# Kernel tuning notes

Measured on AMD Instinct MI355X. Metric: run time of the kernel, lower is better.

The kernel has to match this reference:

```python
import jax, jax.numpy as jnp
import numpy as np

H = 64  # LSTM hidden size (from LSTM(64, ...))

def _lstm(xs, W, U, b, return_sequences):
    """Keras-convention LSTM. xs: [B, T, D]; W: [D, 4H]; U: [H, 4H]; b: [4H].
    Gate order i, f, g(candidate), o; sigmoid recurrent activation, tanh activation."""
    B = xs.shape[0]
    h_dim = U.shape[0]
    # Precompute input projection for all timesteps (hoists the big GEMM out of scan)
    xW = jnp.einsum('btd,dk->btk', xs, W) + b  # [B, T, 4H]

    def step(carry, xw_t):
        h, c = carry
        z = xw_t + h @ U  # [B, 4H]
        i, f, g, o = jnp.split(z, 4, axis=-1)
        i = jax.nn.sigmoid(i)
        f = jax.nn.sigmoid(f)
        g = jnp.tanh(g)
        o = jax.nn.sigmoid(o)
        c = f * c + i * g
        h = o * jnp.tanh(c)
        return (h, c), h

    h0 = jnp.zeros((B, h_dim), xs.dtype)
    (hT, _), hs = jax.lax.scan(step, (h0, h0), jnp.swapaxes(xW, 0, 1))
    if return_sequences:
        return jnp.swapaxes(hs, 0, 1)  # [B, T, H]
    return hT  # [B, H]


def setup_inputs() -> dict:
    key = jax.random.key(0)
    ks = jax.random.split(key, 17)
    T = 16384
    num_actions = 10
    s = lambda *sh: 1.0 / np.sqrt(sh[0])
    d = {}
    d['x'] = jax.random.normal(ks[0], (T, 2), dtype=jnp.float32)
    # LSTM 1: input dim 2 -> 64
    d['W1'] = jax.random.normal(ks[1], (2, 4 * H), jnp.float32) * s(2)
    d['U1'] = jax.random.normal(ks[2], (H, 4 * H), jnp.float32) * s(H)
    d['b1'] = jnp.concatenate([jnp.zeros(H), jnp.ones(H), jnp.zeros(2 * H)]).astype(jnp.float32)  # unit forget bias
    # LSTM 2: 64 -> 64
    d['W2'] = jax.random.normal(ks[3], (H, 4 * H), jnp.float32) * s(H)
    d['U2'] = jax.random.normal(ks[4], (H, 4 * H), jnp.float32) * s(H)
    d['b2'] = jnp.concatenate([jnp.zeros(H), jnp.ones(H), jnp.zeros(2 * H)]).astype(jnp.float32)
    # LSTM 3: 64 -> 64 (last step only)
    d['W3'] = jax.random.normal(ks[5], (H, 4 * H), jnp.float32) * s(H)
    d['U3'] = jax.random.normal(ks[6], (H, 4 * H), jnp.float32) * s(H)
    d['b3'] = jnp.concatenate([jnp.zeros(H), jnp.ones(H), jnp.zeros(2 * H)]).astype(jnp.float32)
    # Dense heads
    d['Wd1'] = jax.random.normal(ks[7], (H, 20), jnp.float32) * s(H)
    d['bd1'] = jnp.zeros((20,), jnp.float32)
    d['Wd2'] = jax.random.normal(ks[8], (20, 20), jnp.float32) * s(20)
    d['bd2'] = jnp.zeros((20,), jnp.float32)
    d['Wl'] = jax.random.normal(ks[9], (20, num_actions), jnp.float32) * s(20)
    d['bl'] = jnp.zeros((num_actions,), jnp.float32)
    return d


def reference(x, W1, U1, b1, W2, U2, b2, W3, U3, b3, Wd1, bd1, Wd2, bd2, Wl, bl):
    # call(): reshape to [1, -1, 2], cast float32
    xs = jnp.reshape(x.astype(jnp.float32), (1, -1, 2))
    h1 = _lstm(xs, W1, U1, b1, return_sequences=True)   # [1, T, 64]
    h2 = _lstm(h1, W2, U2, b2, return_sequences=True)   # [1, T, 64]
    h3 = _lstm(h2, W3, U3, b3, return_sequences=False)  # [1, 64]
    # Dropout layers are identity at inference (no training=True in call())
    h4 = jax.nn.relu(h3 @ Wd1 + bd1)
    h6 = jax.nn.relu(h4 @ Wd2 + bd2)
    logits = h6 @ Wl + bl  # [1, num_actions]
    return logits
```

## Files before the change

### kernel.cpp

```cpp
#include <hip/hip_runtime.h>

#define H 64
#define G4 256
#define CS 128
#define NC 128
#define PB 4
#define TPB (CS / PB)
#define LOG2E 1.44269504088896f

typedef _Float16 f16x8 __attribute__((ext_vector_type(8)));
typedef float f32x4 __attribute__((ext_vector_type(4)));
typedef __fp16 p16x2 __attribute__((ext_vector_type(2)));

union I4F { int4 i; f16x8 h; };

__device__ __forceinline__ int pack_f16s(float lo, float hi, float sc) {
  union { p16x2 h; int i; } u;
  u.h = __builtin_amdgcn_cvt_pkrtz(lo * sc, hi * sc);
  return u.i;
}
__device__ __forceinline__ int pack_f16(float lo, float hi) {
  union { p16x2 h; int i; } u;
  u.h = __builtin_amdgcn_cvt_pkrtz(lo, hi);
  return u.i;
}
__device__ __forceinline__ void wg_barrier() {
  asm volatile("s_waitcnt lgkmcnt(0)\n\ts_barrier" ::: "memory");
}

__global__ __launch_bounds__(G4) void proj_x(const float* __restrict__ x,
                                             const float* __restrict__ W,
                                             const float* __restrict__ b,
                                             float* __restrict__ xw) {
  const int t = blockIdx.x;
  const int j = threadIdx.x;
  const int G = j >> 6, u = j & 63;
  const float sc = (G == 2) ? 2.f * LOG2E : -LOG2E;
  xw[(size_t)t * G4 + u * 4 + G] =
      sc * fmaf(x[2 * t], W[j], fmaf(x[2 * t + 1], W[G4 + j], b[j]));
}

__global__ __attribute__((amdgpu_flat_work_group_size(G4, G4),
                          amdgpu_waves_per_eu(1, 1)))
void pipe_step(int q, const float* __restrict__ xw1,
               const float* __restrict__ U1, const float* __restrict__ U2,
               const float* __restrict__ U3, const float* __restrict__ W2,
               const float* __restrict__ W3, const float* __restrict__ b2,
               const float* __restrict__ b3, __fp16* __restrict__ h1s,
               __fp16* __restrict__ h2s, __fp16* __restrict__ hb3,
               float* __restrict__ xw2s, float* __restrict__ xw3s,
               float* __restrict__ cst, float* __restrict__ h3out, int T) {
  const int bid = (int)blockIdx.x;
  const int tid = (int)threadIdx.x;

  if (bid >= 3) {
    const int p = bid - 3;
    const int lay = p / PB;
    const int pb = p % PB;
    const int chunk = q - 1 - 2 * lay;
    if (chunk < 0 || chunk >= NC) return;
    const __fp16* hsrc = lay ? h2s : h1s;
    const float* Wm = lay ? W3 : W2;
    const float* bb = lay ? b3 : b2;
    float* dst = (lay ? xw3s : xw2s) + (size_t)(chunk & 1) * CS * G4;
    const int tl0 = pb * TPB;

    __shared__ float sh[TPB * H];
    {
      union { int4 i; __fp16 hh[8]; } uu;
      uu.i = ((const int4*)(hsrc + (size_t)(chunk * CS + tl0) * H))[tid];
      float4 lo = make_float4(uu.hh[0], uu.hh[1], uu.hh[2], uu.hh[3]);
      float4 hi = make_float4(uu.hh[4], uu.hh[5], uu.hh[6], uu.hh[7]);
      ((float4*)sh)[2 * tid] = lo;
      ((float4*)sh)[2 * tid + 1] = hi;
    }
    __syncthreads();

    const int j = tid;
    const int G = j >> 6, u = j & 63;
    const int pos = (u << 2) | G;
    const float scl = (G == 2) ? 2.f * LOG2E : -LOG2E;
    float w[H];
#pragma unroll
    for (int k = 0; k < H; ++k) w[k] = Wm[k * G4 + j];
    const float bj = bb[j];

    for (int tt = 0; tt < TPB; ++tt) {
      const float4* h4 = (const float4*)(sh + tt * H);
      float a0 = bj, a1 = 0.f, a2 = 0.f, a3 = 0.f;
#pragma unroll
      for (int kk = 0; kk < H / 4; ++kk) {
        float4 hv = h4[kk];
        a0 = fmaf(hv.x, w[4 * kk + 0], a0);
        a1 = fmaf(hv.y, w[4 * kk + 1], a1);
        a2 = fmaf(hv.z, w[4 * kk + 2], a2);
        a3 = fmaf(hv.w, w[4 * kk + 3], a3);
      }
      dst[(size_t)(tl0 + tt) * G4 + pos] = scl * ((a0 + a1) + (a2 + a3));
    }
    return;
  }

  const int role = bid;
  const int chunk = q - 2 * role;
  if (chunk < 0 || chunk >= NC) return;
  const int t0 = chunk * CS;

  __shared__ int4 sh_h[2][8];

  const int wv = tid >> 6;
  const int n = tid & 15;
  const int kg = (tid & 63) >> 4;
  const int u_own = (wv << 4) | ((n & 3) << 2) | kg;

  const float* U = (role == 0) ? U1 : ((role == 1) ? U2 : U3);
  const float scl = ((n & 3) == 2) ? 2.f * LOG2E : -LOG2E;

  I4F au[4][2];
#pragma unroll
  for (int tau = 0; tau < 4; ++tau) {
    const int colA = ((n & 3) << 6) | (wv << 4) | (tau << 2) | (n >> 2);
#pragma unroll
    for (int kap = 0; kap < 2; ++kap) {
      const int k0 = kap * 32 + kg * 8;
      au[tau][kap].i = make_int4(
          pack_f16s(U[(k0 + 0) * G4 + colA], U[(k0 + 1) * G4 + colA], scl),
          pack_f16s(U[(k0 + 2) * G4 + colA], U[(k0 + 3) * G4 + colA], scl),
          pack_f16s(U[(k0 + 4) * G4 + colA], U[(k0 + 5) * G4 + colA], scl),
          pack_f16s(U[(k0 + 6) * G4 + colA], U[(k0 + 7) * G4 + colA], scl));
      asm volatile("" : "+v"(au[tau][kap].i.x), "+v"(au[tau][kap].i.y),
                       "+v"(au[tau][kap].i.z), "+v"(au[tau][kap].i.w));
    }
  }

  const float* xbase =
      (role == 0) ? (xw1 + (size_t)t0 * G4)
                  : ((role == 1) ? xw2s : xw3s) + (size_t)(chunk & 1) * CS * G4;
  __fp16* hout = (role == 0) ? h1s : h2s;

  float c = (chunk == 0) ? 0.f : cst[role * 64 + u_own];
  if (tid < 8) {
    int4 v = make_int4(0, 0, 0, 0);
    if (chunk > 0) {
      const int4* src = (role == 0)
              ? (const int4*)(h1s + (size_t)(t0 - 1) * H)
              : (role == 1) ? (const int4*)(h2s + (size_t)(t0 - 1) * H)
                            : (const int4*)hb3;
      v = src[tid];
    }
    sh_h[(t0 - 1) & 1][tid] = v;
  }
  wg_barrier();

  const int us0 = (wv << 4) | kg;
  f32x4 sd0, sd1, sd2, sd3;
  {
    const float* r0 = xbase + (size_t)0 * G4;
    sd0 = *(const f32x4*)(r0 + (us0 + 0) * 4);
    sd1 = *(const f32x4*)(r0 + (us0 + 4) * 4);
    sd2 = *(const f32x4*)(r0 + (us0 + 8) * 4);
    sd3 = *(const f32x4*)(r0 + (us0 + 12) * 4);
  }

  for (int tt = 0; tt < CS; ++tt) {
    const int s = t0 + tt;
    I4F b0, b1;
    b0.i = sh_h[(s - 1) & 1][kg];
    b1.i = sh_h[(s - 1) & 1][4 + kg];

    f32x4 a0 = __builtin_amdgcn_mfma_f32_16x16x32_f16(au[0][0].h, b0.h, sd0, 0, 0, 0);
    f32x4 a1 = __builtin_amdgcn_mfma_f32_16x16x32_f16(au[1][0].h, b0.h, sd1, 0, 0, 0);
    f32x4 a2 = __builtin_amdgcn_mfma_f32_16x16x32_f16(au[2][0].h, b0.h, sd2, 0, 0, 0);
    f32x4 a3 = __builtin_amdgcn_mfma_f32_16x16x32_f16(au[3][0].h, b0.h, sd3, 0, 0, 0);
    a0 = __builtin_amdgcn_mfma_f32_16x16x32_f16(au[0][1].h, b1.h, a0, 0, 0, 0);
    a1 = __builtin_amdgcn_mfma_f32_16x16x32_f16(au[1][1].h, b1.h, a1, 0, 0, 0);
    a2 = __builtin_amdgcn_mfma_f32_16x16x32_f16(au[2][1].h, b1.h, a2, 0, 0, 0);
    a3 = __builtin_amdgcn_mfma_f32_16x16x32_f16(au[3][1].h, b1.h, a3, 0, 0, 0);

    const int tn = (tt + 1 < CS) ? (tt + 1) : tt;
    {
      const float* rn = xbase + (size_t)tn * G4;
      sd0 = *(const f32x4*)(rn + (us0 + 0) * 4);
      sd1 = *(const f32x4*)(rn + (us0 + 4) * 4);
      sd2 = *(const f32x4*)(rn + (us0 + 8) * 4);
      sd3 = *(const f32x4*)(rn + (us0 + 12) * 4);
    }

    const bool se = ((n & 1) == 0);
    const bool s01 = ((n & 2) == 0);
    float z0, z1, z2, z3;
    {
      float lo, hi;
      lo = se ? a0[0] : a1[0]; hi = se ? a2[0] : a3[0]; z0 = s01 ? lo : hi;
      lo = se ? a0[1] : a1[1]; hi = se ? a2[1] : a3[1]; z1 = s01 ? lo : hi;
      lo = se ? a0[2] : a1[2]; hi = se ? a2[2] : a3[2]; z2 = s01 ? lo : hi;
      lo = se ? a0[3] : a1[3]; hi = se ? a2[3] : a3[3]; z3 = s01 ? lo : hi;
    }

    const float gi = __builtin_amdgcn_rcpf(1.f + exp2f(z0));
    const float gf = __builtin_amdgcn_rcpf(1.f + exp2f(z1));
    const float gg = fmaf(-2.f, __builtin_amdgcn_rcpf(1.f + exp2f(z2)), 1.f);
    const float go = __builtin_amdgcn_rcpf(1.f + exp2f(z3));
    c = fmaf(gf, c, gi * gg);
    const float th =
        fmaf(-2.f, __builtin_amdgcn_rcpf(1.f + exp2f(c * (2.f * LOG2E))), 1.f);
    const float h = go * th;

    if (n < 4) {
      ((__fp16*)&sh_h[s & 1][0])[u_own] = (__fp16)h;
      if (role < 2) {
        hout[(size_t)s * H + u_own] = (__fp16)h;
      } else {
        if (tt == CS - 1) hb3[u_own] = (__fp16)h;
        if (s == T - 1) h3out[u_own] = h;
      }
      if (tt == CS - 1) cst[role * 64 + u_own] = c;
    }
    wg_barrier();
  }
}

__global__ __launch_bounds__(64) void head_k(const float* __restrict__ hlast,
                                             const float* __restrict__ Wd1,
                                             const float* __restrict__ bd1,
                                             const float* __restrict__ Wd2,
                                             const float* __restrict__ bd2,
                                             const float* __restrict__ Wl,
                                             const float* __restrict__ bl,
                                             float* __restrict__ out) {
  __shared__ float s_h[H];
  __shared__ float s_a[20];
  __shared__ float s_b[20];
  const int j = threadIdx.x;
  s_h[j] = hlast[j];
  __syncthreads();
  if (j < 20) {
    float acc = bd1[j];
#pragma unroll
    for (int k = 0; k < H; ++k) acc = fmaf(s_h[k], Wd1[k * 20 + j], acc);
    s_a[j] = fmaxf(acc, 0.f);
  }
  __syncthreads();
  if (j < 20) {
    float acc = bd2[j];
#pragma unroll
    for (int k = 0; k < 20; ++k) acc = fmaf(s_a[k], Wd2[k * 20 + j], acc);
    s_b[j] = fmaxf(acc, 0.f);
  }
  __syncthreads();
  if (j < 10) {
    float acc = bl[j];
#pragma unroll
    for (int k = 0; k < 20; ++k) acc = fmaf(s_b[k], Wl[k * 10 + j], acc);
    out[j] = acc;
  }
}

extern "C" void kernel_launch(void* const* d_in, const int* in_sizes, int n_in,
                              void* d_out, int out_size, void* d_ws, size_t ws_size,
                              hipStream_t stream) {
  const float* x   = (const float*)d_in[0];
  const float* W1  = (const float*)d_in[1];
  const float* U1  = (const float*)d_in[2];
  const float* b1  = (const float*)d_in[3];
  const float* W2  = (const float*)d_in[4];
  const float* U2  = (const float*)d_in[5];
  const float* b2  = (const float*)d_in[6];
  const float* W3  = (const float*)d_in[7];
  const float* U3  = (const float*)d_in[8];
  const float* b3  = (const float*)d_in[9];
  const float* Wd1 = (const float*)d_in[10];
  const float* bd1 = (const float*)d_in[11];
  const float* Wd2 = (const float*)d_in[12];
  const float* bd2 = (const float*)d_in[13];
  const float* Wl  = (const float*)d_in[14];
  const float* bl  = (const float*)d_in[15];
  const int T = in_sizes[0] / 2;

  float* xw1 = (float*)d_ws;
  __fp16* h1s = (__fp16*)(xw1 + (size_t)T * G4);
  __fp16* h2s = h1s + (size_t)T * H;
  float* xw2s = (float*)(h2s + (size_t)T * H);
  float* xw3s = xw2s + 2 * CS * G4;
  __fp16* hb3 = (__fp16*)(xw3s + 2 * CS * G4);
  float* cst = (float*)(hb3 + H);
  float* h3out = cst + 192;

  proj_x<<<T, G4, 0, stream>>>(x, W1, b1, xw1);
  for (int q = 0; q < NC + 4; ++q) {
    pipe_step<<<3 + 2 * PB, G4, 0, stream>>>(q, xw1, U1, U2, U3, W2, W3, b2,
                                             b3, h1s, h2s, hb3, xw2s, xw3s,
                                             cst, h3out, T);
  }
  head_k<<<1, 64, 0, stream>>>(h3out, Wd1, bd1, Wd2, bd2, Wl, bl,
                               (float*)d_out);
}
```

Baseline: 6.784 ms.

## Shorten per-step LSTM critical path and halve chunk size

Chunk size drops from 128 to 64 steps and the chunk count rises to 256, with fewer pipeline blocks per chunk. This should make the startup and drain of the layer-wavefront pipeline shorter, at the cost of more chunk hand-offs. The two dependent MFMAs per gate tile become independent MFMAs (the second starts from zero) followed by a vector add, which removes a serial MFMA dependency. The cell state is now kept pre-scaled by 2*log2(e) so the tanh exponent needs no extra multiply, and exp2 uses the raw hardware builtin. The loop is also unrolled by 2. The raw exp2 builtin may be less accurate or handle range differently from exp2f, and the new chunk parameters assume the rest of the schedule (cst, xw double buffers) still matches.

```diff
diff --git a/kernel.cpp b/kernel.cpp
--- a/kernel.cpp
+++ b/kernel.cpp
@@ -2,9 +2,9 @@
 
 #define H 64
 #define G4 256
-#define CS 128
-#define NC 128
-#define PB 4
+#define CS 64
+#define NC 256
+#define PB 2
 #define TPB (CS / PB)
 #define LOG2E 1.44269504088896f
 
@@ -138,7 +138,7 @@
                   : ((role == 1) ? xw2s : xw3s) + (size_t)(chunk & 1) * CS * G4;
   __fp16* hout = (role == 0) ? h1s : h2s;
 
-  float c = (chunk == 0) ? 0.f : cst[role * 64 + u_own];
+  float cp = (chunk == 0) ? 0.f : cst[role * 64 + u_own];
   if (tid < 8) {
     int4 v = make_int4(0, 0, 0, 0);
     if (chunk > 0) {
@@ -155,13 +155,16 @@
   const int us0 = (wv << 4) | kg;
   f32x4 sd0, sd1, sd2, sd3;
   {
-    const float* r0 = xbase + (size_t)0 * G4;
+    const float* r0 = xbase;
     sd0 = *(const f32x4*)(r0 + (us0 + 0) * 4);
     sd1 = *(const f32x4*)(r0 + (us0 + 4) * 4);
     sd2 = *(const f32x4*)(r0 + (us0 + 8) * 4);
     sd3 = *(const f32x4*)(r0 + (us0 + 12) * 4);
   }
-
+  f32x4 zero4 = {0.f, 0.f, 0.f, 0.f};
+  asm volatile("" : "+v"(zero4));
+
+#pragma unroll 2
   for (int tt = 0; tt < CS; ++tt) {
     const int s = t0 + tt;
     I4F b0, b1;
@@ -172,10 +175,11 @@
     f32x4 a1 = __builtin_amdgcn_mfma_f32_16x16x32_f16(au[1][0].h, b0.h, sd1, 0, 0, 0);
     f32x4 a2 = __builtin_amdgcn_mfma_f32_16x16x32_f16(au[2][0].h, b0.h, sd2, 0, 0, 0);
     f32x4 a3 = __builtin_amdgcn_mfma_f32_16x16x32_f16(au[3][0].h, b0.h, sd3, 0, 0, 0);
-    a0 = __builtin_amdgcn_mfma_f32_16x16x32_f16(au[0][1].h, b1.h, a0, 0, 0, 0);
-    a1 = __builtin_amdgcn_mfma_f32_16x16x32_f16(au[1][1].h, b1.h, a1, 0, 0, 0);
-    a2 = __builtin_amdgcn_mfma_f32_16x16x32_f16(au[2][1].h, b1.h, a2, 0, 0, 0);
-    a3 = __builtin_amdgcn_mfma_f32_16x16x32_f16(au[3][1].h, b1.h, a3, 0, 0, 0);
+    f32x4 c0 = __builtin_amdgcn_mfma_f32_16x16x32_f16(au[0][1].h, b1.h, zero4, 0, 0, 0);
+    f32x4 c1 = __builtin_amdgcn_mfma_f32_16x16x32_f16(au[1][1].h, b1.h, zero4, 0, 0, 0);
+    f32x4 c2 = __builtin_amdgcn_mfma_f32_16x16x32_f16(au[2][1].h, b1.h, zero4, 0, 0, 0);
+    f32x4 c3 = __builtin_amdgcn_mfma_f32_16x16x32_f16(au[3][1].h, b1.h, zero4, 0, 0, 0);
+    a0 = a0 + c0; a1 = a1 + c1; a2 = a2 + c2; a3 = a3 + c3;
 
     const int tn = (tt + 1 < CS) ? (tt + 1) : tt;
     {
@@ -197,14 +201,19 @@
       lo = se ? a0[3] : a1[3]; hi = se ? a2[3] : a3[3]; z3 = s01 ? lo : hi;
     }
 
-    const float gi = __builtin_amdgcn_rcpf(1.f + exp2f(z0));
-    const float gf = __builtin_amdgcn_rcpf(1.f + exp2f(z1));
-    const float gg = fmaf(-2.f, __builtin_amdgcn_rcpf(1.f + exp2f(z2)), 1.f);
-    const float go = __builtin_amdgcn_rcpf(1.f + exp2f(z3));
-    c = fmaf(gf, c, gi * gg);
-    const float th =
-        fmaf(-2.f, __builtin_amdgcn_rcpf(1.f + exp2f(c * (2.f * LOG2E))), 1.f);
-    const float h = go * th;
+    const float e0 = __builtin_amdgcn_exp2f(z0);
+    const float e1 = __builtin_amdgcn_exp2f(z1);
+    const float e2 = __builtin_amdgcn_exp2f(z2);
+    const float e3 = __builtin_amdgcn_exp2f(z3);
+    const float gi = __builtin_amdgcn_rcpf(1.f + e0);
+    const float gf = __builtin_amdgcn_rcpf(1.f + e1);
+    const float r2 = __builtin_amdgcn_rcpf(1.f + e2);
+    const float go = __builtin_amdgcn_rcpf(1.f + e3);
+    const float ggs = fmaf(-4.f * LOG2E, r2, 2.f * LOG2E);
+    cp = fmaf(gf, cp, gi * ggs);
+    const float go2 = go + go;
+    const float r3 = __builtin_amdgcn_rcpf(1.f + __builtin_amdgcn_exp2f(cp));
+    const float h = fmaf(-go2, r3, go);
 
     if (n < 4) {
       ((__fp16*)&sh_h[s & 1][0])[u_own] = (__fp16)h;
@@ -214,7 +223,7 @@
         if (tt == CS - 1) hb3[u_own] = (__fp16)h;
         if (s == T - 1) h3out[u_own] = h;
       }
-      if (tt == CS - 1) cst[role * 64 + u_own] = c;
+      if (tt == CS - 1) cst[role * 64 + u_own] = cp;
     }
     wg_barrier();
   }
```

Result: faster. 6.629 ms (-2.3%).
